# Performance work log

Measured on AMD Instinct MI355X. Metric: run time of the kernel, lower is better.

The kernel has to match this reference:

```python
import jax, jax.numpy as jnp
import numpy as np

N_U, N_B = 100000, 50000
SU, SB = 256, 256
D0, D1, KF = 64, 128, 64
E_U, E_B, Q = 1000000, 500000, 100000
R_MIN, R_MAX = 1.0, 5.0


def setup_inputs() -> dict:
    key = jax.random.key(0)
    ks = jax.random.split(key, 24)
    f = lambda k, s: jax.random.normal(k, s, jnp.float32)
    inp = {
        "S_u": f(ks[0], (N_U, SU)),
        "S_b": f(ks[1], (N_B, SB)),
        "edge_index_u": jax.random.randint(ks[2], (2, E_U), 0, N_U, jnp.int32),
        "edge_index_b0": jax.random.randint(ks[3], (2, E_B), 0, N_B, jnp.int32),
        "edge_index_b1": jax.random.randint(ks[4], (2, E_B), 0, N_B, jnp.int32),
        "edge_index_b2": jax.random.randint(ks[5], (2, E_B), 0, N_B, jnp.int32),
        "user_idx": jax.random.randint(ks[6], (Q,), 0, N_U, jnp.int32),
        "biz_idx": jax.random.randint(ks[7], (Q,), 0, N_B, jnp.int32),
        # parameters (torch Linear weight [out,in] stored transposed as [in,out])
        "W1_u": f(ks[8], (SU, D0)) * 0.05,
        "W1_b": f(ks[9], (SB, D0)) * 0.05,
        "a_u": f(ks[10], (2 * D0,)) * 0.1,
        "a_b": f(ks[11], (2 * D0,)) * 0.1,
        "omega": jnp.ones((3,), jnp.float32) / 3.0,
        "W2_u": f(ks[12], (D0, D1)) * 0.05,
        "W2_us": f(ks[13], (SU, D1)) * 0.05,
        "b1_u": jnp.zeros((D1,), jnp.float32),
        "W2_b": f(ks[14], (D0, D1)) * 0.05,
        "W2_bs": f(ks[15], (SB, D1)) * 0.05,
        "b1_b": jnp.zeros((D1,), jnp.float32),
        "W3_u": f(ks[16], (D1, KF)) * 0.05,
        "W3_b": f(ks[17], (D1, KF)) * 0.05,
        "H4_u": f(ks[18], (N_U, KF)) * 0.01,
        "H4_b": f(ks[19], (N_B, KF)) * 0.01,
        "bias_u": jnp.zeros((N_U,), jnp.float32),
        "bias_b": jnp.zeros((N_B,), jnp.float32),
        "bias_global": jnp.zeros((), jnp.float32),
    }
    return inp


def _leaky(x):
    return jnp.where(x >= 0, x, 0.2 * x)


def _softmax_by_dst(e, dst, n, mask=None):
    # segment softmax over edges grouped by destination node
    e_for_max = e if mask is None else jnp.where(mask, e, -jnp.inf)
    emax = jax.ops.segment_max(e_for_max, dst, num_segments=n)
    safe = jnp.where(jnp.isfinite(emax), emax, 0.0)
    e_exp = jnp.exp(e - safe[dst])
    if mask is not None:
        e_exp = e_exp * mask.astype(e.dtype)
    s = jax.ops.segment_sum(e_exp, dst, num_segments=n)
    return e_exp / (s[dst] + 1e-16)


def reference(S_u, S_b, edge_index_u, edge_index_b0, edge_index_b1, edge_index_b2,
              user_idx, biz_idx, W1_u, W1_b, a_u, a_b, omega, W2_u, W2_us, b1_u,
              W2_b, W2_bs, b1_b, W3_u, W3_b, H4_u, H4_b, bias_u, bias_b, bias_global):
    H1_u = S_u @ W1_u  # [N_U, D0]
    H1_b = S_b @ W1_b  # [N_B, D0]

    # --- user graph attention: e = leaky(a[:D0].H1[dst] + a[D0:].H1[src]) ---
    src_u, dst_u = edge_index_u[0], edge_index_u[1]
    el_u = H1_u @ a_u[:D0]
    er_u = H1_u @ a_u[D0:]
    e_u = _leaky(el_u[dst_u] + er_u[src_u])
    alpha_u = _softmax_by_dst(e_u, dst_u, N_U)
    H2_u = jax.ops.segment_sum(H1_u[src_u] * alpha_u[:, None], dst_u, num_segments=N_U)

    # --- multi-graph biz attention: merge duplicate (src,dst) across graphs ---
    om = jax.nn.softmax(omega)
    el_b = H1_b @ a_b[:D0]
    er_b = H1_b @ a_b[D0:]
    eis = (edge_index_b0, edge_index_b1, edge_index_b2)
    srcs = jnp.concatenate([ei[0] for ei in eis])
    dsts = jnp.concatenate([ei[1] for ei in eis])
    e_b = jnp.concatenate([om[g] * (el_b[ei[1]] + er_b[ei[0]]) for g, ei in enumerate(eis)])
    # sort by (src, dst) so duplicate edges are adjacent (fixed-shape torch.unique)
    order = jnp.lexsort((dsts, srcs))
    ss, ds, es = srcs[order], dsts[order], e_b[order]
    is_first = jnp.concatenate([jnp.ones((1,), bool), (ss[1:] != ss[:-1]) | (ds[1:] != ds[:-1])])
    gid = jnp.cumsum(is_first) - 1  # group id per edge
    E_tot = ss.shape[0]
    group_e = jax.ops.segment_sum(es, gid, num_segments=E_tot)
    me = _leaky(group_e[gid])  # merged, leaky-relu'd score, replicated per duplicate
    alpha_b = _softmax_by_dst(me, ds, N_B, mask=is_first)  # duplicates get alpha=0
    H2_b = jax.ops.segment_sum(H1_b[ss] * alpha_b[:, None], ds, num_segments=N_B)

    # --- layer 2 + latent factors ---
    H3_u = jax.nn.elu(H2_u @ W2_u + S_u @ W2_us + b1_u)
    H3_b = jax.nn.elu(H2_b @ W2_b + S_b @ W2_bs + b1_b)
    U_all = jax.nn.relu(H3_u @ W3_u) + H4_u
    B_all = jax.nn.relu(H3_b @ W3_b) + H4_b

    logit = (jnp.sum(U_all[user_idx] * B_all[biz_idx], axis=1)
             + bias_u[user_idx] + bias_b[biz_idx] + bias_global)
    pred = (R_MAX - R_MIN) * jax.nn.sigmoid(logit) + R_MIN
    return pred, U_all, B_all
```

## Files before the change

kernel.cpp:

```cpp
#include <hip/hip_runtime.h>
#include <math.h>

__device__ __forceinline__ float leakyf(float x) { return x >= 0.f ? x : 0.2f * x; }

__device__ __forceinline__ unsigned short f2bf(float f) {
    unsigned u = __float_as_uint(f);
    u += 0x7FFFu + ((u >> 16) & 1u);
    return (unsigned short)(u >> 16);
}
__device__ __forceinline__ float bf2f(unsigned short h) {
    return __uint_as_float(((unsigned)h) << 16);
}
__device__ __forceinline__ unsigned pack2(float a, float b) {
    return ((unsigned)f2bf(b) << 16) | f2bf(a);
}

typedef __attribute__((ext_vector_type(8))) short bf16x8;
typedef __attribute__((ext_vector_type(4))) float f32x4;

#define PP 16
#define CAPU 96
#define CAPB 80

struct PrepArgs {
    const float *Su, *Sb;
    unsigned short *Subf, *Sbbf;
    const float* win[8];
    unsigned short* wout[8];
    const float* omega; float* om;
    int* zp[4]; int zn[4];
    int gcu, gcb, gz, nu4, nb4;
};

__global__ __launch_bounds__(256) void prep_all(PrepArgs P)
{
    int b = blockIdx.x, tid = threadIdx.x;
    if (b < P.gcu) {
        int i = b * 256 + tid;
        if (i < P.nu4) {
            float4 v = ((const float4*)P.Su)[i];
            ushort4 o; o.x = f2bf(v.x); o.y = f2bf(v.y); o.z = f2bf(v.z); o.w = f2bf(v.w);
            ((ushort4*)P.Subf)[i] = o;
        }
        return;
    }
    b -= P.gcu;
    if (b < P.gcb) {
        int i = b * 256 + tid;
        if (i < P.nb4) {
            float4 v = ((const float4*)P.Sb)[i];
            ushort4 o; o.x = f2bf(v.x); o.y = f2bf(v.y); o.z = f2bf(v.z); o.w = f2bf(v.w);
            ((ushort4*)P.Sbbf)[i] = o;
        }
        return;
    }
    b -= P.gcb;
    if (b < P.gz) {
        int base = b * 1024 + tid * 4;
#pragma unroll
        for (int j = 0; j < 4; ++j) {
            int id = base + j;
            int a = 0;
            while (a < 4 && id >= P.zn[a]) { id -= P.zn[a]; ++a; }
            if (a < 4) P.zp[a][id] = 0;
        }
        return;
    }
    b -= P.gz;
    const int KS[8] = {256, 256, 256, 256, 64, 64, 128, 128};
    const int NS[8] = {64, 64, 128, 128, 128, 128, 64, 64};
    const int BL[8] = {64, 64, 128, 128, 32, 32, 32, 32};
#pragma unroll
    for (int w = 0; w < 8; ++w) {
        if (b < BL[w]) {
            int idx = b * 256 + tid;
            int K = KS[w], N = NS[w];
            int k = idx / N, n = idx % N;
            P.wout[w][(((n >> 4) * (K >> 3) + (k >> 3)) << 7) + ((n & 15) << 3) + (k & 7)] =
                f2bf(P.win[w][idx]);
            return;
        }
        b -= BL[w];
    }
    if (tid == 0) {
        float m = fmaxf(P.omega[0], fmaxf(P.omega[1], P.omega[2]));
        float e0 = expf(P.omega[0] - m), e1 = expf(P.omega[1] - m), e2 = expf(P.omega[2] - m);
        float s = e0 + e1 + e2;
        P.om[0] = e0 / s; P.om[1] = e1 / s; P.om[2] = e2 / s;
    }
}

__global__ __launch_bounds__(256) void gemm_s1(
    const unsigned short* __restrict__ A,
    const unsigned short* __restrict__ W1f,
    const unsigned short* __restrict__ W2f,
    const float* __restrict__ avec,
    float* __restrict__ el, float* __restrict__ er,
    unsigned short* __restrict__ H1,
    unsigned short* __restrict__ T,
    int M)
{
    const int lane = threadIdx.x & 63;
    const int wid  = threadIdx.x >> 6;
    const int row0 = (blockIdx.x * 4 + wid) * 16;
    if (row0 >= M) return;
    const int lr = lane & 15, lk = lane >> 4;
    f32x4 acc1[4] = {};
    f32x4 acc2[8] = {};
    const unsigned short* Ap = A + (size_t)(row0 + lr) * 256 + lk * 8;
    const unsigned short* B1 = W1f + ((size_t)lk * 16 + lr) * 8;
    const unsigned short* B2 = W2f + ((size_t)lk * 16 + lr) * 8;
    for (int k0 = 0; k0 < 256; k0 += 32) {
        bf16x8 af = *(const bf16x8*)(Ap + k0);
#pragma unroll
        for (int nb = 0; nb < 4; ++nb) {
            bf16x8 bfr = *(const bf16x8*)(B1 + (size_t)(nb * 32 + (k0 >> 3)) * 128);
            acc1[nb] = __builtin_amdgcn_mfma_f32_16x16x32_bf16(af, bfr, acc1[nb], 0, 0, 0);
        }
#pragma unroll
        for (int nb = 0; nb < 8; ++nb) {
            bf16x8 bfr = *(const bf16x8*)(B2 + (size_t)(nb * 32 + (k0 >> 3)) * 128);
            acc2[nb] = __builtin_amdgcn_mfma_f32_16x16x32_bf16(af, bfr, acc2[nb], 0, 0, 0);
        }
    }
    float pl[4] = {0, 0, 0, 0}, ph[4] = {0, 0, 0, 0};
#pragma unroll
    for (int nb = 0; nb < 4; ++nb) {
        int col = nb * 16 + lr;
        float al = avec[col], ah = avec[64 + col];
#pragma unroll
        for (int j = 0; j < 4; ++j) {
            H1[(size_t)(row0 + lk * 4 + j) * 64 + col] = f2bf(acc1[nb][j]);
            pl[j] += acc1[nb][j] * al;
            ph[j] += acc1[nb][j] * ah;
        }
    }
#pragma unroll
    for (int j = 0; j < 4; ++j) {
#pragma unroll
        for (int s = 8; s; s >>= 1) {
            pl[j] += __shfl_xor(pl[j], s, 16);
            ph[j] += __shfl_xor(ph[j], s, 16);
        }
    }
    if (lr == 0) {
#pragma unroll
        for (int j = 0; j < 4; ++j) {
            el[row0 + lk * 4 + j] = pl[j];
            er[row0 + lk * 4 + j] = ph[j];
        }
    }
#pragma unroll
    for (int nb = 0; nb < 8; ++nb) {
        int col = nb * 16 + lr;
#pragma unroll
        for (int j = 0; j < 4; ++j)
            T[(size_t)(row0 + lk * 4 + j) * 128 + col] = f2bf(acc2[nb][j]);
    }
}

template <int N, int EPI>
__global__ __launch_bounds__(256) void gemm2_mfma(
    const unsigned short* A1, const unsigned short* Wf1, const void* X1, const float* bias1,
    void* C1, int M1, int g1,
    const unsigned short* A2, const unsigned short* Wf2, const void* X2, const float* bias2,
    void* C2, int M2, int K)
{
    const unsigned short *A, *Wf; const void* Xv; const float* bias; void* Cv; int M, bb;
    if ((int)blockIdx.x < g1) { A = A1; Wf = Wf1; Xv = X1; bias = bias1; Cv = C1; M = M1; bb = blockIdx.x; }
    else { A = A2; Wf = Wf2; Xv = X2; bias = bias2; Cv = C2; M = M2; bb = blockIdx.x - g1; }

    const int lane = threadIdx.x & 63;
    const int wid = threadIdx.x >> 6;
    const int row0 = (bb * 4 + wid) * 16;
    if (row0 >= M) return;
    constexpr int NT = N / 16;
    const int lr = lane & 15;
    const int lk = lane >> 4;

    f32x4 acc[NT] = {};
    const unsigned short* Ap = A + (size_t)(row0 + lr) * K + lk * 8;
    const unsigned short* Bp = Wf + ((size_t)lk * 16 + lr) * 8;

    for (int k0 = 0; k0 < K; k0 += 32) {
        bf16x8 af = *(const bf16x8*)(Ap + k0);
#pragma unroll
        for (int nb = 0; nb < NT; ++nb) {
            bf16x8 bfr = *(const bf16x8*)(Bp + (size_t)(nb * (K >> 3) + (k0 >> 3)) * 128);
            acc[nb] = __builtin_amdgcn_mfma_f32_16x16x32_bf16(af, bfr, acc[nb], 0, 0, 0);
        }
    }
#pragma unroll
    for (int nb = 0; nb < NT; ++nb) {
        int col = nb * 16 + lr;
#pragma unroll
        for (int j = 0; j < 4; ++j) {
            int row = row0 + lk * 4 + j;
            size_t o = (size_t)row * N + col;
            float v = acc[nb][j];
            if (EPI == 1) {
                float t = v + bf2f(((const unsigned short*)Xv)[o]) + bias[col];
                ((unsigned short*)Cv)[o] = f2bf(t > 0.f ? t : expm1f(t));
            } else {
                ((float*)Cv)[o] = (v > 0.f ? v : 0.f) + ((const float*)Xv)[o];
            }
        }
    }
}

__global__ __launch_bounds__(256) void app_all(
    const int* __restrict__ ei_u, int EU, int* __restrict__ fill2u, unsigned* __restrict__ bufu,
    const int* __restrict__ e0, const int* __restrict__ e1, const int* __restrict__ e2,
    int EB, int* __restrict__ fill2b, unsigned* __restrict__ bufb,
    int gu)
{
    if ((int)blockIdx.x < gu) {
        int lb = blockIdx.x;
        int e = lb * 256 + threadIdx.x;
        if (e >= EU) return;
        int p = lb & (PP - 1);
        unsigned src = (unsigned)ei_u[e], dst = (unsigned)ei_u[EU + e];
        int cidx = (int)(dst >> 6) * PP + p;
        int pos = atomicAdd(&fill2u[cidx], 1);
        if (pos < CAPU) bufu[(size_t)cidx * CAPU + pos] = ((dst & 63u) << 26) | src;
    } else {
        int lb = blockIdx.x - gu;
        int t = lb * 256 + threadIdx.x;
        if (t >= 3 * EB) return;
        int p = lb & (PP - 1);
        int g = t < EB ? 0 : (t < 2 * EB ? 1 : 2);
        int e = t - g * EB;
        const int* ei = (g == 0) ? e0 : ((g == 1) ? e1 : e2);
        unsigned src = (unsigned)ei[e], dst = (unsigned)ei[EB + e];
        int cidx = (int)(dst >> 4) * PP + p;
        int pos = atomicAdd(&fill2b[cidx], 1);
        if (pos < CAPB) bufb[(size_t)cidx * CAPB + pos] = ((dst & 15u) << 26) | ((unsigned)g << 24) | src;
    }
}

__global__ __launch_bounds__(256) void bin_all(
    const unsigned* __restrict__ bufu, const int* __restrict__ fill2u,
    int* __restrict__ outu, int* __restrict__ rowpu, int* __restrict__ cntu, int NU, int nbku,
    const unsigned* __restrict__ bufb, const int* __restrict__ fill2b,
    int* __restrict__ outb, int* __restrict__ rowpb, int* __restrict__ cntb, int NB, int nbkb,
    int* __restrict__ dupfb)
{
    __shared__ unsigned se[PP * CAPU];
    __shared__ int h[64], hp[64], fo[PP + 1], dupl[64];
    __shared__ unsigned hk[2048];
    const unsigned* buf; const int* fill2; int N, ndpb, CAP, mode, b;
    int *outp, *rowp, *cnt;
    if ((int)blockIdx.x < nbku) {
        b = blockIdx.x; buf = bufu; fill2 = fill2u;
        outp = outu; rowp = rowpu; cnt = cntu; N = NU; ndpb = 64; CAP = CAPU; mode = 0;
    } else {
        b = blockIdx.x - nbku; buf = bufb; fill2 = fill2b;
        outp = outb; rowp = rowpb; cnt = cntb; N = NB; ndpb = 16; CAP = CAPB; mode = 1;
    }
    int tid = threadIdx.x;
    if (tid == 0) {
        int run = 0;
        for (int p = 0; p < PP; ++p) {
            fo[p] = run;
            int f = fill2[b * PP + p];
            if (f > CAP) f = CAP;
            run += f;
        }
        fo[PP] = run;
    }
    if (tid < ndpb) { h[tid] = 0; dupl[tid] = 0; }
    __syncthreads();
    int n = fo[PP];
    for (int idx = tid; idx < PP * CAP; idx += 256) {
        int p = idx / CAP, i = idx - p * CAP;
        if (i < fo[p + 1] - fo[p]) se[fo[p] + i] = buf[(size_t)(b * PP + p) * CAP + i];
    }
    __syncthreads();
    for (int i = tid; i < n; i += 256) atomicAdd(&h[se[i] >> 26], 1);
    __syncthreads();
    if (tid == 0) {
        int run = 0;
        for (int dd = 0; dd < ndpb; ++dd) { hp[dd] = run; run += h[dd]; }
    }
    __syncthreads();
    int outbase = b * PP * CAP;
    if (tid < ndpb && b * ndpb + tid < N) {
        rowp[b * ndpb + tid] = outbase + hp[tid];
        cnt[b * ndpb + tid] = h[tid];
    }
    __syncthreads();
    for (int i = tid; i < n; i += 256) {
        unsigned pay = se[i];
        int pos = atomicAdd(&hp[pay >> 26], 1);
        int v = (mode == 0) ? (int)(pay & 0xFFFFFFu)
                            : (int)((pay & 0xFFFFu) | (((pay >> 24) & 3u) << 16));
        outp[outbase + pos] = v;
    }
    if (mode == 1) {
        for (int i = tid; i < 2048; i += 256) hk[i] = 0xFFFFFFFFu;
        __syncthreads();
        for (int i = tid; i < n; i += 256) {
            unsigned pay = se[i];
            unsigned key = ((pay >> 26) << 16) | (pay & 0xFFFFu);
            unsigned hh = (key * 2654435761u) >> 21;
            while (true) {
                unsigned old = atomicCAS(&hk[hh], 0xFFFFFFFFu, key);
                if (old == 0xFFFFFFFFu) break;
                if (old == key) { dupl[pay >> 26] = 1; break; }
                hh = (hh + 1) & 2047u;
            }
        }
        __syncthreads();
        if (tid < ndpb && b * ndpb + tid < N) dupfb[b * ndpb + tid] = dupl[tid];
    }
}

__global__ __launch_bounds__(256) void gather_all(
    const int* __restrict__ rowpu, const int* __restrict__ cntu, const int* __restrict__ ssrcu,
    const float* __restrict__ elu, const float* __restrict__ eru,
    const unsigned short* __restrict__ H1u, unsigned short* __restrict__ H2u, int NU, int gu,
    const int* __restrict__ rowpb, const int* __restrict__ cntb, const int* __restrict__ spayb,
    const float* __restrict__ om,
    const float* __restrict__ elb, const float* __restrict__ erb,
    const unsigned short* __restrict__ H1b, unsigned short* __restrict__ H2b, int NB,
    const int* __restrict__ dupfb)
{
    int tid = threadIdx.x, lane = tid & 63, wid = tid >> 6;
    int half = lane >> 5, fl = lane & 31;

    if ((int)blockIdx.x < gu) {
        int d = blockIdx.x * 4 + wid;
        if (d >= NU) return;
        int start = rowpu[d], L = cntu[d];
        float eld = elu[d];
        if (L <= 64) {
            int src = -1;
            float p = 0.f;
            if (lane < L) {
                src = ssrcu[start + lane];
                p = expf(leakyf(eld + eru[src]));
            }
            float den = p;
#pragma unroll
            for (int s = 32; s; s >>= 1) den += __shfl_xor(den, s, 64);
            float ax = 0.f, ay = 0.f;
            for (int k = half; k < L; k += 2) {
                float pk = __shfl(p, k, 64);
                int sk = __shfl(src, k, 64);
                unsigned hh = *(const unsigned*)(H1u + (size_t)sk * 64 + fl * 2);
                ax += pk * bf2f((unsigned short)(hh & 0xFFFF));
                ay += pk * bf2f((unsigned short)(hh >> 16));
            }
            ax += __shfl_xor(ax, 32, 64);
            ay += __shfl_xor(ay, 32, 64);
            if (lane < 32) {
                float r = 1.f / (den + 1e-16f);
                *(unsigned*)(H2u + (size_t)d * 64 + fl * 2) = pack2(ax * r, ay * r);
            }
        } else {
            float ax = 0.f, ay = 0.f, den = 0.f;
            for (int i = half; i < L; i += 2) {
                int s = ssrcu[start + i];
                float p = expf(leakyf(eld + eru[s]));
                den += p;
                unsigned hh = *(const unsigned*)(H1u + (size_t)s * 64 + fl * 2);
                ax += p * bf2f((unsigned short)(hh & 0xFFFF));
                ay += p * bf2f((unsigned short)(hh >> 16));
            }
            ax += __shfl_xor(ax, 32, 64);
            ay += __shfl_xor(ay, 32, 64);
            den += __shfl_xor(den, 32, 64);
            if (lane < 32) {
                float r = 1.f / (den + 1e-16f);
                *(unsigned*)(H2u + (size_t)d * 64 + fl * 2) = pack2(ax * r, ay * r);
            }
        }
        return;
    }

    int d = (blockIdx.x - gu) * 4 + wid;
    if (d >= NB) return;
    int start = rowpb[d], L = cntb[d];
    float eld = elb[d];
    float w0 = om[0], w1 = om[1], w2 = om[2];

    if (L <= 64) {
        int src = -1;
        float p = 0.f;
        if (!dupfb[d]) {
            if (lane < L) {
                int pay = spayb[start + lane];
                src = pay & 0xFFFF;
                int g = (unsigned)pay >> 16;
                float w = g == 0 ? w0 : (g == 1 ? w1 : w2);
                p = expf(leakyf(w * (eld + erb[src])));
            }
        } else {
            float w = 0.f;
            if (lane < L) {
                int pay = spayb[start + lane];
                src = pay & 0xFFFF;
                int g = (unsigned)pay >> 16;
                w = g == 0 ? w0 : (g == 1 ? w1 : w2);
            }
            float W = 0.f;
            bool first = (lane < L);
            for (int k = 0; k < L; ++k) {
                int sk = __shfl(src, k, 64);
                float wk = __shfl(w, k, 64);
                if (sk == src && lane < L) {
                    W += wk;
                    if (k < lane) first = false;
                }
            }
            p = first ? expf(leakyf(W * (eld + erb[src]))) : 0.f;
        }
        float den = p;
#pragma unroll
        for (int s = 32; s; s >>= 1) den += __shfl_xor(den, s, 64);
        float ax = 0.f, ay = 0.f;
        for (int k = half; k < L; k += 2) {
            float pk = __shfl(p, k, 64);
            if (pk != 0.f) {
                int sk = __shfl(src, k, 64);
                unsigned hh = *(const unsigned*)(H1b + (size_t)sk * 64 + fl * 2);
                ax += pk * bf2f((unsigned short)(hh & 0xFFFF));
                ay += pk * bf2f((unsigned short)(hh >> 16));
            }
        }
        ax += __shfl_xor(ax, 32, 64);
        ay += __shfl_xor(ay, 32, 64);
        if (lane < 32) {
            float r = 1.f / (den + 1e-16f);
            *(unsigned*)(H2b + (size_t)d * 64 + fl * 2) = pack2(ax * r, ay * r);
        }
    } else {
        float accs = 0.f, den = 0.f;
        for (int i = start; i < start + L; ++i) {
            int pi = spayb[i];
            int si = pi & 0xFFFF;
            float W = 0.f;
            bool first = true;
            for (int j = start + lane; j < start + L; j += 64) {
                int pj = spayb[j];
                if ((pj & 0xFFFF) == si) {
                    int g = (unsigned)pj >> 16;
                    W += g == 0 ? w0 : (g == 1 ? w1 : w2);
                    if (j < i) first = false;
                }
            }
#pragma unroll
            for (int s = 32; s; s >>= 1) W += __shfl_xor(W, s, 64);
            first = __all(first);
            if (first) {
                float pp = expf(leakyf(W * (eld + erb[si])));
                den += pp;
                accs += pp * bf2f(H1b[(size_t)si * 64 + lane]);
            }
        }
        H2b[(size_t)d * 64 + lane] = f2bf(accs / (den + 1e-16f));
    }
}

__global__ __launch_bounds__(256) void pred_k(
    const int* __restrict__ uidx, const int* __restrict__ bidx,
    const float* __restrict__ U, const float* __restrict__ B,
    const float* __restrict__ bu, const float* __restrict__ bb,
    const float* __restrict__ bg, float* __restrict__ pred, int Q)
{
    int g = blockIdx.x * 8 + (threadIdx.x >> 5);
    int fl = threadIdx.x & 31;
    if (g >= Q) return;
    int u = uidx[g], b = bidx[g];
    float2 uv = *(const float2*)(U + (size_t)u * 64 + fl * 2);
    float2 bv = *(const float2*)(B + (size_t)b * 64 + fl * 2);
    float p = uv.x * bv.x + uv.y * bv.y;
#pragma unroll
    for (int s = 16; s; s >>= 1) p += __shfl_xor(p, s, 32);
    if (fl == 0) {
        float logit = p + bu[u] + bb[b] + bg[0];
        float sg = 1.f / (1.f + expf(-logit));
        pred[g] = 4.f * sg + 1.f;
    }
}

extern "C" void kernel_launch(void* const* d_in, const int* in_sizes, int n_in,
                              void* d_out, int out_size, void* d_ws, size_t ws_size,
                              hipStream_t stream)
{
    const float* S_u   = (const float*)d_in[0];
    const float* S_b   = (const float*)d_in[1];
    const int* ei_u    = (const int*)d_in[2];
    const int* ei_b0   = (const int*)d_in[3];
    const int* ei_b1   = (const int*)d_in[4];
    const int* ei_b2   = (const int*)d_in[5];
    const int* uidx    = (const int*)d_in[6];
    const int* bidx    = (const int*)d_in[7];
    const float* W1_u  = (const float*)d_in[8];
    const float* W1_b  = (const float*)d_in[9];
    const float* a_u   = (const float*)d_in[10];
    const float* a_b   = (const float*)d_in[11];
    const float* omega = (const float*)d_in[12];
    const float* W2_u  = (const float*)d_in[13];
    const float* W2_us = (const float*)d_in[14];
    const float* b1_u  = (const float*)d_in[15];
    const float* W2_b  = (const float*)d_in[16];
    const float* W2_bs = (const float*)d_in[17];
    const float* b1_b  = (const float*)d_in[18];
    const float* W3_u  = (const float*)d_in[19];
    const float* W3_b  = (const float*)d_in[20];
    const float* H4_u  = (const float*)d_in[21];
    const float* H4_b  = (const float*)d_in[22];
    const float* bias_u = (const float*)d_in[23];
    const float* bias_b = (const float*)d_in[24];
    const float* bias_g = (const float*)d_in[25];

    const int NU = in_sizes[0] / 256;
    const int NB = in_sizes[1] / 256;
    const int EU = in_sizes[2] / 2;
    const int EB = in_sizes[3] / 2;
    const int Q  = in_sizes[6];

    float* out  = (float*)d_out;
    float* pred = out;
    float* Uo   = out + Q;
    float* Bo   = Uo + (size_t)NU * 64;

    char* wsp = (char*)d_ws;
    size_t off = 0;
    auto carve = [&](size_t bytes) -> void* {
        void* p = wsp + off;
        off += (bytes + 255) & ~(size_t)255;
        return p;
    };
    unsigned short* Subf = (unsigned short*)carve((size_t)NU * 256 * 2);
    unsigned short* Sbbf = (unsigned short*)carve((size_t)NB * 256 * 2);
    unsigned short* H3u  = Subf;
    unsigned short* H3b  = Sbbf;
    unsigned short* H1u  = (unsigned short*)carve((size_t)NU * 64 * 2);
    unsigned short* H1b  = (unsigned short*)carve((size_t)NB * 64 * 2);
    unsigned short* Tu   = (unsigned short*)carve((size_t)NU * 128 * 2);
    unsigned short* Tb   = (unsigned short*)carve((size_t)NB * 128 * 2);
    unsigned short* H2u  = (unsigned short*)carve((size_t)NU * 64 * 2);
    unsigned short* H2b  = (unsigned short*)carve((size_t)NB * 64 * 2);
    float* el_u = (float*)carve((size_t)NU * 4);
    float* er_u = (float*)carve((size_t)NU * 4);
    float* el_b = (float*)carve((size_t)NB * 4);
    float* er_b = (float*)carve((size_t)NB * 4);
    const int nbk_u = (NU + 63) >> 6;
    const int nbk_b = (NB + 15) >> 4;
    const int n2_u = nbk_u * PP;
    const int n2_b = nbk_b * PP;
    int* fill2_u = (int*)carve((size_t)n2_u * 4);
    int* fill2_b = (int*)carve((size_t)n2_b * 4);
    unsigned* buf_u = (unsigned*)carve((size_t)n2_u * CAPU * 4);
    unsigned* buf_b = (unsigned*)carve((size_t)n2_b * CAPB * 4);
    int* ssrc_u  = (int*)carve((size_t)n2_u * CAPU * 4);
    int* spay_b  = (int*)carve((size_t)n2_b * CAPB * 4);
    int* rowp_u  = (int*)carve((size_t)NU * 4);
    int* cnt_u   = (int*)carve((size_t)NU * 4);
    int* rowp_b  = (int*)carve((size_t)NB * 4);
    int* cnt_b   = (int*)carve((size_t)NB * 4);
    int* dupf_b  = (int*)carve((size_t)NB * 4);
    float* om    = (float*)carve(256);
    unsigned short* w1u_s  = (unsigned short*)carve((size_t)256 * 64 * 2);
    unsigned short* w1b_s  = (unsigned short*)carve((size_t)256 * 64 * 2);
    unsigned short* w2us_s = (unsigned short*)carve((size_t)256 * 128 * 2);
    unsigned short* w2bs_s = (unsigned short*)carve((size_t)256 * 128 * 2);
    unsigned short* w2u_s  = (unsigned short*)carve((size_t)64 * 128 * 2);
    unsigned short* w2b_s  = (unsigned short*)carve((size_t)64 * 128 * 2);
    unsigned short* w3u_s  = (unsigned short*)carve((size_t)128 * 64 * 2);
    unsigned short* w3b_s  = (unsigned short*)carve((size_t)128 * 64 * 2);
    (void)ws_size; (void)n_in; (void)out_size;

    dim3 b256(256);

    PrepArgs P;
    P.Su = S_u; P.Sb = S_b; P.Subf = Subf; P.Sbbf = Sbbf;
    const float* wins[8] = {W1_u, W1_b, W2_us, W2_bs, W2_u, W2_b, W3_u, W3_b};
    unsigned short* wouts[8] = {w1u_s, w1b_s, w2us_s, w2bs_s, w2u_s, w2b_s, w3u_s, w3b_s};
    for (int i = 0; i < 8; ++i) { P.win[i] = wins[i]; P.wout[i] = wouts[i]; }
    P.omega = omega; P.om = om;
    P.zp[0] = fill2_u; P.zn[0] = n2_u;
    P.zp[1] = fill2_b; P.zn[1] = n2_b;
    P.zp[2] = fill2_b; P.zn[2] = 0;
    P.zp[3] = fill2_b; P.zn[3] = 0;
    P.nu4 = NU * 64; P.nb4 = NB * 64;
    P.gcu = (P.nu4 + 255) / 256;
    P.gcb = (P.nb4 + 255) / 256;
    const int ztot = n2_u + n2_b;
    P.gz = (ztot + 1023) / 1024;
    const int gswz = 64 + 64 + 128 + 128 + 32 + 32 + 32 + 32;
    prep_all<<<dim3(P.gcu + P.gcb + P.gz + gswz + 1), b256, 0, stream>>>(P);

    gemm_s1<<<dim3((NU / 16 + 3) / 4), b256, 0, stream>>>(
        Subf, w1u_s, w2us_s, a_u, el_u, er_u, H1u, Tu, NU);
    gemm_s1<<<dim3((NB / 16 + 3) / 4), b256, 0, stream>>>(
        Sbbf, w1b_s, w2bs_s, a_b, el_b, er_b, H1b, Tb, NB);

    const int gu_cnt = (EU + 255) / 256;
    const int gb_cnt = (3 * EB + 255) / 256;
    app_all<<<dim3(gu_cnt + gb_cnt), b256, 0, stream>>>(
        ei_u, EU, fill2_u, buf_u,
        ei_b0, ei_b1, ei_b2, EB, fill2_b, buf_b, gu_cnt);

    bin_all<<<dim3(nbk_u + nbk_b), b256, 0, stream>>>(
        buf_u, fill2_u, ssrc_u, rowp_u, cnt_u, NU, nbk_u,
        buf_b, fill2_b, spay_b, rowp_b, cnt_b, NB, nbk_b, dupf_b);

    const int gu_g = (NU + 3) / 4;
    const int gb_g = (NB + 3) / 4;
    gather_all<<<dim3(gu_g + gb_g), b256, 0, stream>>>(
        rowp_u, cnt_u, ssrc_u, el_u, er_u, H1u, H2u, NU, gu_g,
        rowp_b, cnt_b, spay_b, om, el_b, er_b, H1b, H2b, NB, dupf_b);

    const int g1a = (NU / 16 + 3) / 4;
    const int g2a = (NB / 16 + 3) / 4;
    gemm2_mfma<128, 1><<<dim3(g1a + g2a), b256, 0, stream>>>(
        H2u, w2u_s, Tu, b1_u, H3u, NU, g1a,
        H2b, w2b_s, Tb, b1_b, H3b, NB, 64);
    gemm2_mfma<64, 2><<<dim3(g1a + g2a), b256, 0, stream>>>(
        H3u, w3u_s, H4_u, nullptr, Uo, NU, g1a,
        H3b, w3b_s, H4_b, nullptr, Bo, NB, 128);

    pred_k<<<dim3((Q + 7) / 8), b256, 0, stream>>>(uidx, bidx, Uo, Bo, bias_u, bias_b, bias_g, pred, Q);
}
```

Measured before the change: 454.1 us.

## Pre-sort edges per block in shared memory before appending to coarser buckets

The edge bucketing now has each block load 2048 edges, histogram them into coarse destination groups (256 users or 128 businesses) in shared memory, and reserve space with one global atomic per group. Payloads are then written contiguously into the reserved slots. This replaces one global atomic per edge with one per nonempty group per block, and shrinks the bin stage grid to fewer, larger blocks with a bigger dedup hash table. The risks are capacity overflow of the per-partition buffers (512/672 slots), more serial per-bucket copy loops, and higher shared memory use in bin_all, which lowers occupancy.

```diff
diff --git a/kernel.cpp b/kernel.cpp
--- a/kernel.cpp
+++ b/kernel.cpp
@@ -18,9 +18,11 @@
 typedef __attribute__((ext_vector_type(8))) short bf16x8;
 typedef __attribute__((ext_vector_type(4))) float f32x4;
 
-#define PP 16
-#define CAPU 96
-#define CAPB 80
+#define PPG 8
+#define BATCH 2048
+#define NBGMAX 392
+#define CAPPU 512
+#define CAPPB 672
 
 struct PrepArgs {
     const float *Su, *Sb;
@@ -28,7 +30,7 @@
     const float* win[8];
     unsigned short* wout[8];
     const float* omega; float* om;
-    int* zp[4]; int zn[4];
+    int* zp[2]; int zn[2];
     int gcu, gcb, gz, nu4, nb4;
 };
 
@@ -56,13 +58,12 @@
     }
     b -= P.gcb;
     if (b < P.gz) {
-        int base = b * 1024 + tid * 4;
+        int id = b * 1024 + tid * 4;
 #pragma unroll
         for (int j = 0; j < 4; ++j) {
-            int id = base + j;
-            int a = 0;
-            while (a < 4 && id >= P.zn[a]) { id -= P.zn[a]; ++a; }
-            if (a < 4) P.zp[a][id] = 0;
+            int i = id + j;
+            if (i < P.zn[0]) P.zp[0][i] = 0;
+            else if (i - P.zn[0] < P.zn[1]) P.zp[1][i - P.zn[0]] = 0;
         }
         return;
     }
@@ -209,105 +210,159 @@
 }
 
 __global__ __launch_bounds__(256) void app_all(
-    const int* __restrict__ ei_u, int EU, int* __restrict__ fill2u, unsigned* __restrict__ bufu,
+    const int* __restrict__ ei_u, int EU, int* __restrict__ fillu, unsigned* __restrict__ bufu, int nbgu,
     const int* __restrict__ e0, const int* __restrict__ e1, const int* __restrict__ e2,
-    int EB, int* __restrict__ fill2b, unsigned* __restrict__ bufb,
+    int EB, int* __restrict__ fillb, unsigned* __restrict__ bufb, int nbgb,
     int gu)
 {
-    if ((int)blockIdx.x < gu) {
-        int lb = blockIdx.x;
-        int e = lb * 256 + threadIdx.x;
-        if (e >= EU) return;
-        int p = lb & (PP - 1);
-        unsigned src = (unsigned)ei_u[e], dst = (unsigned)ei_u[EU + e];
-        int cidx = (int)(dst >> 6) * PP + p;
-        int pos = atomicAdd(&fill2u[cidx], 1);
-        if (pos < CAPU) bufu[(size_t)cidx * CAPU + pos] = ((dst & 63u) << 26) | src;
+    __shared__ int bh[NBGMAX], bs[NBGMAX], bc[NBGMAX], gb[NBGMAX];
+    __shared__ unsigned sp[BATCH];
+    int tid = threadIdx.x;
+    const bool isU = (int)blockIdx.x < gu;
+    int lb = isU ? blockIdx.x : blockIdx.x - gu;
+    int p = lb & (PPG - 1);
+    int nbg = isU ? nbgu : nbgb;
+    int CAP = isU ? CAPPU : CAPPB;
+    int* fill = isU ? fillu : fillb;
+    unsigned* buf = isU ? bufu : bufb;
+    int base = lb * BATCH;
+    int tot = isU ? EU : 3 * EB;
+
+    for (int i = tid; i < nbg; i += 256) bh[i] = 0;
+    __syncthreads();
+
+    bool ok[8]; int bkt[8]; unsigned pay[8];
+#pragma unroll
+    for (int i = 0; i < 8; ++i) {
+        int t = base + i * 256 + tid;
+        ok[i] = t < tot;
+        bkt[i] = 0; pay[i] = 0;
+        if (ok[i]) {
+            if (isU) {
+                unsigned src = (unsigned)ei_u[t], dst = (unsigned)ei_u[EU + t];
+                bkt[i] = (int)(dst >> 8);
+                pay[i] = ((dst & 255u) << 17) | src;
+            } else {
+                int g = t < EB ? 0 : (t < 2 * EB ? 1 : 2);
+                int e = t - g * EB;
+                const int* ei = (g == 0) ? e0 : ((g == 1) ? e1 : e2);
+                unsigned src = (unsigned)ei[e], dst = (unsigned)ei[EB + e];
+                bkt[i] = (int)(dst >> 7);
+                pay[i] = ((dst & 127u) << 18) | ((unsigned)g << 16) | src;
+            }
+            atomicAdd(&bh[bkt[i]], 1);
+        }
+    }
+    __syncthreads();
+    if (tid == 0) {
+        int run = 0;
+        for (int b = 0; b < nbg; ++b) { bs[b] = run; run += bh[b]; }
+    }
+    __syncthreads();
+    for (int b = tid; b < nbg; b += 256) {
+        bc[b] = bs[b];
+        if (bh[b] > 0) gb[b] = atomicAdd(&fill[b * PPG + p], bh[b]);
+    }
+    __syncthreads();
+#pragma unroll
+    for (int i = 0; i < 8; ++i) {
+        if (ok[i]) {
+            int pos = atomicAdd(&bc[bkt[i]], 1);
+            sp[pos] = pay[i];
+        }
+    }
+    __syncthreads();
+    for (int b = tid; b < nbg; b += 256) {
+        int c = bh[b];
+        if (c == 0) continue;
+        int s = bs[b], g0 = gb[b];
+        unsigned* dst = buf + (size_t)(b * PPG + p) * CAP;
+        for (int j = 0; j < c; ++j) {
+            int gp = g0 + j;
+            if (gp < CAP) dst[gp] = sp[s + j];
+        }
+    }
+}
+
+__global__ __launch_bounds__(256) void bin_all(
+    const unsigned* __restrict__ bufu, const int* __restrict__ fillu,
+    int* __restrict__ outu, int* __restrict__ rowpu, int* __restrict__ cntu, int NU, int nbgu,
+    const unsigned* __restrict__ bufb, const int* __restrict__ fillb,
+    int* __restrict__ outb, int* __restrict__ rowpb, int* __restrict__ cntb, int NB, int nbgb,
+    int* __restrict__ dupfb)
+{
+    __shared__ unsigned se[PPG * CAPPB];
+    __shared__ int h[256], hp[256], fo[PPG + 1], dupl[128];
+    __shared__ unsigned hk[8192];
+    const unsigned* buf; const int* fill; int N, ndpb, CAP, mode, b;
+    int *outp, *rowp, *cnt;
+    if ((int)blockIdx.x < nbgu) {
+        b = blockIdx.x; buf = bufu; fill = fillu;
+        outp = outu; rowp = rowpu; cnt = cntu; N = NU; ndpb = 256; CAP = CAPPU; mode = 0;
     } else {
-        int lb = blockIdx.x - gu;
-        int t = lb * 256 + threadIdx.x;
-        if (t >= 3 * EB) return;
-        int p = lb & (PP - 1);
-        int g = t < EB ? 0 : (t < 2 * EB ? 1 : 2);
-        int e = t - g * EB;
-        const int* ei = (g == 0) ? e0 : ((g == 1) ? e1 : e2);
-        unsigned src = (unsigned)ei[e], dst = (unsigned)ei[EB + e];
-        int cidx = (int)(dst >> 4) * PP + p;
-        int pos = atomicAdd(&fill2b[cidx], 1);
-        if (pos < CAPB) bufb[(size_t)cidx * CAPB + pos] = ((dst & 15u) << 26) | ((unsigned)g << 24) | src;
-    }
-}
-
-__global__ __launch_bounds__(256) void bin_all(
-    const unsigned* __restrict__ bufu, const int* __restrict__ fill2u,
-    int* __restrict__ outu, int* __restrict__ rowpu, int* __restrict__ cntu, int NU, int nbku,
-    const unsigned* __restrict__ bufb, const int* __restrict__ fill2b,
-    int* __restrict__ outb, int* __restrict__ rowpb, int* __restrict__ cntb, int NB, int nbkb,
-    int* __restrict__ dupfb)
-{
-    __shared__ unsigned se[PP * CAPU];
-    __shared__ int h[64], hp[64], fo[PP + 1], dupl[64];
-    __shared__ unsigned hk[2048];
-    const unsigned* buf; const int* fill2; int N, ndpb, CAP, mode, b;
-    int *outp, *rowp, *cnt;
-    if ((int)blockIdx.x < nbku) {
-        b = blockIdx.x; buf = bufu; fill2 = fill2u;
-        outp = outu; rowp = rowpu; cnt = cntu; N = NU; ndpb = 64; CAP = CAPU; mode = 0;
-    } else {
-        b = blockIdx.x - nbku; buf = bufb; fill2 = fill2b;
-        outp = outb; rowp = rowpb; cnt = cntb; N = NB; ndpb = 16; CAP = CAPB; mode = 1;
+        b = blockIdx.x - nbgu; buf = bufb; fill = fillb;
+        outp = outb; rowp = rowpb; cnt = cntb; N = NB; ndpb = 128; CAP = CAPPB; mode = 1;
     }
     int tid = threadIdx.x;
     if (tid == 0) {
         int run = 0;
-        for (int p = 0; p < PP; ++p) {
+        for (int p = 0; p < PPG; ++p) {
             fo[p] = run;
-            int f = fill2[b * PP + p];
+            int f = fill[b * PPG + p];
             if (f > CAP) f = CAP;
             run += f;
         }
-        fo[PP] = run;
-    }
-    if (tid < ndpb) { h[tid] = 0; dupl[tid] = 0; }
-    __syncthreads();
-    int n = fo[PP];
-    for (int idx = tid; idx < PP * CAP; idx += 256) {
+        fo[PPG] = run;
+    }
+    if (tid < ndpb) h[tid] = 0;
+    if (tid < 128) dupl[tid] = 0;
+    __syncthreads();
+    int n = fo[PPG];
+    for (int idx = tid; idx < PPG * CAP; idx += 256) {
         int p = idx / CAP, i = idx - p * CAP;
-        if (i < fo[p + 1] - fo[p]) se[fo[p] + i] = buf[(size_t)(b * PP + p) * CAP + i];
-    }
-    __syncthreads();
-    for (int i = tid; i < n; i += 256) atomicAdd(&h[se[i] >> 26], 1);
+        if (i < fo[p + 1] - fo[p]) se[fo[p] + i] = buf[(size_t)(b * PPG + p) * CAP + i];
+    }
+    __syncthreads();
+    if (mode == 0) {
+        for (int i = tid; i < n; i += 256) atomicAdd(&h[se[i] >> 17], 1);
+    } else {
+        for (int i = tid; i < n; i += 256) atomicAdd(&h[se[i] >> 18], 1);
+    }
     __syncthreads();
     if (tid == 0) {
         int run = 0;
         for (int dd = 0; dd < ndpb; ++dd) { hp[dd] = run; run += h[dd]; }
     }
     __syncthreads();
-    int outbase = b * PP * CAP;
+    int outbase = b * PPG * CAP;
     if (tid < ndpb && b * ndpb + tid < N) {
         rowp[b * ndpb + tid] = outbase + hp[tid];
         cnt[b * ndpb + tid] = h[tid];
     }
     __syncthreads();
-    for (int i = tid; i < n; i += 256) {
-        unsigned pay = se[i];
-        int pos = atomicAdd(&hp[pay >> 26], 1);
-        int v = (mode == 0) ? (int)(pay & 0xFFFFFFu)
-                            : (int)((pay & 0xFFFFu) | (((pay >> 24) & 3u) << 16));
-        outp[outbase + pos] = v;
-    }
-    if (mode == 1) {
-        for (int i = tid; i < 2048; i += 256) hk[i] = 0xFFFFFFFFu;
+    if (mode == 0) {
+        for (int i = tid; i < n; i += 256) {
+            unsigned pay = se[i];
+            int pos = atomicAdd(&hp[pay >> 17], 1);
+            outp[outbase + pos] = (int)(pay & 0x1FFFFu);
+        }
+    } else {
+        for (int i = tid; i < n; i += 256) {
+            unsigned pay = se[i];
+            int pos = atomicAdd(&hp[pay >> 18], 1);
+            outp[outbase + pos] = (int)(pay & 0x3FFFFu);
+        }
+        for (int i = tid; i < 8192; i += 256) hk[i] = 0xFFFFFFFFu;
         __syncthreads();
         for (int i = tid; i < n; i += 256) {
             unsigned pay = se[i];
-            unsigned key = ((pay >> 26) << 16) | (pay & 0xFFFFu);
-            unsigned hh = (key * 2654435761u) >> 21;
+            unsigned key = ((pay >> 18) << 16) | (pay & 0xFFFFu);
+            unsigned hh = (key * 2654435761u) >> 19;
             while (true) {
                 unsigned old = atomicCAS(&hk[hh], 0xFFFFFFFFu, key);
                 if (old == 0xFFFFFFFFu) break;
-                if (old == key) { dupl[pay >> 26] = 1; break; }
-                hh = (hh + 1) & 2047u;
+                if (old == key) { dupl[pay >> 18] = 1; break; }
+                hh = (hh + 1) & 8191u;
             }
         }
         __syncthreads();
@@ -547,16 +602,14 @@
     float* er_u = (float*)carve((size_t)NU * 4);
     float* el_b = (float*)carve((size_t)NB * 4);
     float* er_b = (float*)carve((size_t)NB * 4);
-    const int nbk_u = (NU + 63) >> 6;
-    const int nbk_b = (NB + 15) >> 4;
-    const int n2_u = nbk_u * PP;
-    const int n2_b = nbk_b * PP;
-    int* fill2_u = (int*)carve((size_t)n2_u * 4);
-    int* fill2_b = (int*)carve((size_t)n2_b * 4);
-    unsigned* buf_u = (unsigned*)carve((size_t)n2_u * CAPU * 4);
-    unsigned* buf_b = (unsigned*)carve((size_t)n2_b * CAPB * 4);
-    int* ssrc_u  = (int*)carve((size_t)n2_u * CAPU * 4);
-    int* spay_b  = (int*)carve((size_t)n2_b * CAPB * 4);
+    const int nbg_u = (NU + 255) >> 8;
+    const int nbg_b = (NB + 127) >> 7;
+    int* fill_u = (int*)carve((size_t)nbg_u * PPG * 4);
+    int* fill_b = (int*)carve((size_t)nbg_b * PPG * 4);
+    unsigned* buf_u = (unsigned*)carve((size_t)nbg_u * PPG * CAPPU * 4);
+    unsigned* buf_b = (unsigned*)carve((size_t)nbg_b * PPG * CAPPB * 4);
+    int* ssrc_u  = (int*)carve((size_t)nbg_u * PPG * CAPPU * 4);
+    int* spay_b  = (int*)carve((size_t)nbg_b * PPG * CAPPB * 4);
     int* rowp_u  = (int*)carve((size_t)NU * 4);
     int* cnt_u   = (int*)carve((size_t)NU * 4);
     int* rowp_b  = (int*)carve((size_t)NB * 4);
@@ -581,14 +634,12 @@
     unsigned short* wouts[8] = {w1u_s, w1b_s, w2us_s, w2bs_s, w2u_s, w2b_s, w3u_s, w3b_s};
     for (int i = 0; i < 8; ++i) { P.win[i] = wins[i]; P.wout[i] = wouts[i]; }
     P.omega = omega; P.om = om;
-    P.zp[0] = fill2_u; P.zn[0] = n2_u;
-    P.zp[1] = fill2_b; P.zn[1] = n2_b;
-    P.zp[2] = fill2_b; P.zn[2] = 0;
-    P.zp[3] = fill2_b; P.zn[3] = 0;
+    P.zp[0] = fill_u; P.zn[0] = nbg_u * PPG;
+    P.zp[1] = fill_b; P.zn[1] = nbg_b * PPG;
     P.nu4 = NU * 64; P.nb4 = NB * 64;
     P.gcu = (P.nu4 + 255) / 256;
     P.gcb = (P.nb4 + 255) / 256;
-    const int ztot = n2_u + n2_b;
+    const int ztot = nbg_u * PPG + nbg_b * PPG;
     P.gz = (ztot + 1023) / 1024;
     const int gswz = 64 + 64 + 128 + 128 + 32 + 32 + 32 + 32;
     prep_all<<<dim3(P.gcu + P.gcb + P.gz + gswz + 1), b256, 0, stream>>>(P);
@@ -598,15 +649,15 @@
     gemm_s1<<<dim3((NB / 16 + 3) / 4), b256, 0, stream>>>(
         Sbbf, w1b_s, w2bs_s, a_b, el_b, er_b, H1b, Tb, NB);
 
-    const int gu_cnt = (EU + 255) / 256;
-    const int gb_cnt = (3 * EB + 255) / 256;
-    app_all<<<dim3(gu_cnt + gb_cnt), b256, 0, stream>>>(
-        ei_u, EU, fill2_u, buf_u,
-        ei_b0, ei_b1, ei_b2, EB, fill2_b, buf_b, gu_cnt);
-
-    bin_all<<<dim3(nbk_u + nbk_b), b256, 0, stream>>>(
-        buf_u, fill2_u, ssrc_u, rowp_u, cnt_u, NU, nbk_u,
-        buf_b, fill2_b, spay_b, rowp_b, cnt_b, NB, nbk_b, dupf_b);
+    const int gu_app = (EU + BATCH - 1) / BATCH;
+    const int gb_app = (3 * EB + BATCH - 1) / BATCH;
+    app_all<<<dim3(gu_app + gb_app), b256, 0, stream>>>(
+        ei_u, EU, fill_u, buf_u, nbg_u,
+        ei_b0, ei_b1, ei_b2, EB, fill_b, buf_b, nbg_b, gu_app);
+
+    bin_all<<<dim3(nbg_u + nbg_b), b256, 0, stream>>>(
+        buf_u, fill_u, ssrc_u, rowp_u, cnt_u, NU, nbg_u,
+        buf_b, fill_b, spay_b, rowp_b, cnt_b, NB, nbg_b, dupf_b);
 
     const int gu_g = (NU + 3) / 4;
     const int gb_g = (NB + 3) / 4;
```

After: 401.8 us. 1.13x faster.
